# Performance work log

Measured on AMD Instinct MI355X. Metric: run time of the kernel, lower is better.

Reference implementation:

```python
import jax, jax.numpy as jnp
import numpy as np

B, N, C, H = 1, 512, 128, 128  # batch, tokens, pair channels, hidden
ENDING = False
EPS = 1e-5


def _ln(x, w, b):
    m = jnp.mean(x, axis=-1, keepdims=True)
    v = jnp.var(x, axis=-1, keepdims=True)
    return (x - m) * jax.lax.rsqrt(v + EPS) * w + b


def setup_inputs() -> dict:
    key = jax.random.key(0)
    ks = jax.random.split(key, 5)
    s = 0.02  # weight init scale
    return {
        "x": jax.random.normal(ks[0], (B, N, N, C), jnp.float32),
        "norm_in_w": jnp.ones((C,), jnp.float32),
        "norm_in_b": jnp.zeros((C,), jnp.float32),
        "p_in_w": jax.random.normal(ks[1], (2 * H, C), jnp.float32) * s,
        "g_in_w": jax.random.normal(ks[2], (2 * H, C), jnp.float32) * s,
        "norm_out_w": jnp.ones((H,), jnp.float32),
        "norm_out_b": jnp.zeros((H,), jnp.float32),
        "p_out_w": jax.random.normal(ks[3], (C, H), jnp.float32) * s,
        "g_out_w": jax.random.normal(ks[4], (C, C), jnp.float32) * s,
    }


def reference(x, norm_in_w, norm_in_b, p_in_w, g_in_w,
              norm_out_w, norm_out_b, p_out_w, g_out_w):
    # x: [B, N, N, C]
    xn = _ln(x, norm_in_w, norm_in_b)                       # [B,N,N,C]
    h = (xn @ p_in_w.T) * jax.nn.sigmoid(xn @ g_in_w.T)     # [B,N,N,2H]
    a, b = h[..., :H], h[..., H:]
    if ENDING:  # incoming edges
        t = jnp.einsum('bkid,bkjd->bijd', a, b)
    else:       # outgoing edges
        t = jnp.einsum('bikd,bjkd->bijd', a, b)             # [B,N,N,H]
    on = _ln(t, norm_out_w, norm_out_b)
    # NOTE: output gate uses the *input* layernorm activations (xn), per source
    return (on @ p_out_w.T) * jax.nn.sigmoid(xn @ g_out_w.T)  # [B,N,N,C]
```

## Files before the change

### kernel.cpp

```cpp
#include <hip/hip_runtime.h>

typedef short short8 __attribute__((ext_vector_type(8)));
typedef _Float16 half8 __attribute__((ext_vector_type(8)));
typedef float f32x4 __attribute__((ext_vector_type(4)));
typedef unsigned short u16;

#define MFMA16H(a,b,c) __builtin_amdgcn_mfma_f32_16x16x32_f16((a),(b),(c),0,0,0)

__device__ __forceinline__ u16 f2h(float f){
  _Float16 h = (_Float16)f;
  return __builtin_bit_cast(u16, h);
}
__device__ __forceinline__ float h2f(u16 u){
  _Float16 h = __builtin_bit_cast(_Float16, u);
  return (float)h;
}
__device__ __forceinline__ float sigmoidf_(float x){
  return 1.0f / (1.0f + __expf(-x));
}
__device__ __forceinline__ half8 ldh8(const u16* p){ return *(const half8*)p; }

#define PLANE 262144

__global__ __launch_bounds__(256) void prep_w(
    const float* __restrict__ p_in, const float* __restrict__ g_in,
    const float* __restrict__ p_out, const float* __restrict__ g_out,
    u16* __restrict__ wbuf)
{
  int idx = blockIdx.x * 256 + threadIdx.x;
  float v;
  if (idx < 32768)       v = p_in[idx];
  else if (idx < 65536)  v = g_in[idx - 32768];
  else if (idx < 81920)  v = p_out[idx - 65536];
  else                   v = g_out[idx - 81920];
  wbuf[idx] = f2h(v);
}

template<bool S>
__global__ __launch_bounds__(256) void stage1(
    const float* __restrict__ x,
    const float* __restrict__ niw, const float* __restrict__ nib,
    const u16* __restrict__ wbuf,
    u16* __restrict__ a_h, u16* __restrict__ a_l,
    u16* __restrict__ b_h, u16* __restrict__ b_l,
    u16* __restrict__ gate)
{
  __shared__ __align__(16) u16 xnT[64*136];
  __shared__ __align__(16) u16 wp [64*136];
  __shared__ __align__(16) u16 wg [64*136];
  __shared__ __align__(16) u16 hTh[64*72];
  __shared__ __align__(16) u16 hTl[64*72];

  int t = threadIdx.x;
  int p0 = blockIdx.x * 64;
  int i_row = p0 >> 9, k0 = p0 & 511;

  {
    int px = t >> 2, part = t & 3;
    const float* xr = x + (size_t)(p0 + px) * 128 + part * 32;
    float v[32];
    float s = 0.f, ss = 0.f;
#pragma unroll
    for (int q = 0; q < 8; ++q) {
      float4 f = *(const float4*)(xr + q * 4);
      v[q*4+0] = f.x; v[q*4+1] = f.y; v[q*4+2] = f.z; v[q*4+3] = f.w;
      s  += f.x + f.y + f.z + f.w;
      ss += f.x*f.x + f.y*f.y + f.z*f.z + f.w*f.w;
    }
    s  += __shfl_xor(s, 1);  s  += __shfl_xor(s, 2);
    ss += __shfl_xor(ss, 1); ss += __shfl_xor(ss, 2);
    float m  = s * (1.f/128.f);
    float var = ss * (1.f/128.f) - m*m;
    float rs = rsqrtf(var + 1e-5f);
#pragma unroll
    for (int q = 0; q < 4; ++q) {
      short8 o;
#pragma unroll
      for (int j = 0; j < 8; ++j) {
        int c = part*32 + q*8 + j;
        float xv = (v[q*8+j] - m) * rs * niw[c] + nib[c];
        o[j] = (short)f2h(xv);
      }
      *(short8*)&xnT[px*136 + part*32 + q*8] = o;
    }
  }
  __syncthreads();

  int wave = t >> 6, lane = t & 63;
  int fr = lane & 15, hi = lane >> 4;
  int m0 = wave * 16;

  half8 afr[4];
#pragma unroll
  for (int kk = 0; kk < 4; ++kk)
    afr[kk] = ldh8(&xnT[(m0 + fr)*136 + kk*32 + hi*8]);

  for (int ns = 0; ns < 6; ++ns) {
    __syncthreads();
    if (ns < 4) {
      int n0 = ns * 64;
#pragma unroll
      for (int q = 0; q < 4; ++q) {
        int c = t + q*256;
        int row = c >> 4, ko = (c & 15) * 8;
        *(short8*)&wp[row*136 + ko] = *(const short8*)&wbuf[n0*128 + row*128 + ko];
        *(short8*)&wg[row*136 + ko] = *(const short8*)&wbuf[32768 + n0*128 + row*128 + ko];
      }
    } else {
      int n0 = (ns - 4) * 64;
#pragma unroll
      for (int q = 0; q < 4; ++q) {
        int c = t + q*256;
        int row = c >> 4, ko = (c & 15) * 8;
        *(short8*)&wp[row*136 + ko] = *(const short8*)&wbuf[81920 + n0*128 + row*128 + ko];
      }
    }
    __syncthreads();

    f32x4 accP[4] = {}, accG[4] = {};
#pragma unroll
    for (int kk = 0; kk < 4; ++kk) {
#pragma unroll
      for (int nf = 0; nf < 4; ++nf) {
        half8 bp = ldh8(&wp[(nf*16 + fr)*136 + kk*32 + hi*8]);
        accP[nf] = MFMA16H(afr[kk], bp, accP[nf]);
        if (ns < 4) {
          half8 bg = ldh8(&wg[(nf*16 + fr)*136 + kk*32 + hi*8]);
          accG[nf] = MFMA16H(afr[kk], bg, accG[nf]);
        }
      }
    }

    if (ns < 4) {
#pragma unroll
      for (int nf = 0; nf < 4; ++nf) {
#pragma unroll
        for (int r = 0; r < 4; ++r) {
          float h = accP[nf][r] * sigmoidf_(accG[nf][r]);
          int nl = nf*16 + fr;
          int pl = m0 + hi*4 + r;
          u16 hh = f2h(h);
          hTh[nl*72 + pl] = hh;
          if constexpr (S) {
            hTl[nl*72 + pl] = f2h(h - h2f(hh));
          }
        }
      }
      __syncthreads();
      int n0 = ns * 64;
      u16* dh = (ns < 2) ? a_h : b_h;
      u16* dl = (ns < 2) ? a_l : b_l;
      int dbase = (ns < 2) ? n0 : n0 - 128;
      int nl = t >> 2, po = (t & 3) * 16;
      size_t g = (size_t)(dbase + nl) * PLANE + (size_t)i_row * 512 + k0 + po;
      *(short8*)&dh[g]     = *(const short8*)&hTh[nl*72 + po];
      *(short8*)&dh[g + 8] = *(const short8*)&hTh[nl*72 + po + 8];
      if constexpr (S) {
        *(short8*)&dl[g]     = *(const short8*)&hTl[nl*72 + po];
        *(short8*)&dl[g + 8] = *(const short8*)&hTl[nl*72 + po + 8];
      }
    } else {
      int n0 = (ns - 4) * 64;
#pragma unroll
      for (int nf = 0; nf < 4; ++nf) {
#pragma unroll
        for (int r = 0; r < 4; ++r) {
          float gv = sigmoidf_(accP[nf][r]);
          int cc = n0 + nf*16 + fr;
          int pl = m0 + hi*4 + r;
          gate[(size_t)(p0 + pl)*128 + cc] = f2h(gv);
        }
      }
    }
  }
}

template<bool S>
__global__ __launch_bounds__(256) void stage2(
    const u16* __restrict__ a_h, const u16* __restrict__ a_l,
    const u16* __restrict__ b_h, const u16* __restrict__ b_l,
    u16* __restrict__ t_h, u16* __restrict__ t_l)
{
  int bid = blockIdx.x;
  int d  = bid >> 4;
  int it = (bid >> 2) & 3;
  int jt = bid & 3;
  size_t abase = (size_t)d * PLANE + (size_t)it * 128 * 512;
  size_t bbase = (size_t)d * PLANE + (size_t)jt * 128 * 512;

  __shared__ __align__(16) u16 Ash[128*72], Bsh[128*72];
  __shared__ __align__(16) u16 Asl[128*72], Bsl[128*72];

  int t = threadIdx.x, wave = t >> 6, lane = t & 63;
  int fr = lane & 15, hi = lane >> 4;
  int m0 = (wave & 1) * 64, n0 = (wave >> 1) * 64;
  int srow = t >> 1, sko = (t & 1) * 32;

  f32x4 acc[4][4] = {};

  for (int step = 0; step < 8; ++step) {
    __syncthreads();
    int kb = step * 64;
#pragma unroll
    for (int q = 0; q < 4; ++q) {
      size_t go = (size_t)srow*512 + kb + sko + q*8;
      *(short8*)&Ash[srow*72 + sko + q*8] = *(const short8*)&a_h[abase + go];
      *(short8*)&Bsh[srow*72 + sko + q*8] = *(const short8*)&b_h[bbase + go];
      if constexpr (S) {
        *(short8*)&Asl[srow*72 + sko + q*8] = *(const short8*)&a_l[abase + go];
        *(short8*)&Bsl[srow*72 + sko + q*8] = *(const short8*)&b_l[bbase + go];
      }
    }
    __syncthreads();
#pragma unroll
    for (int kk = 0; kk < 2; ++kk) {
      half8 afh[4], bfh[4], afl[4], bfl[4];
#pragma unroll
      for (int mf = 0; mf < 4; ++mf) {
        afh[mf] = ldh8(&Ash[(m0 + mf*16 + fr)*72 + kk*32 + hi*8]);
        if constexpr (S) afl[mf] = ldh8(&Asl[(m0 + mf*16 + fr)*72 + kk*32 + hi*8]);
      }
#pragma unroll
      for (int nf = 0; nf < 4; ++nf) {
        bfh[nf] = ldh8(&Bsh[(n0 + nf*16 + fr)*72 + kk*32 + hi*8]);
        if constexpr (S) bfl[nf] = ldh8(&Bsl[(n0 + nf*16 + fr)*72 + kk*32 + hi*8]);
      }
#pragma unroll
      for (int mf = 0; mf < 4; ++mf)
#pragma unroll
        for (int nf = 0; nf < 4; ++nf) {
          acc[mf][nf] = MFMA16H(afh[mf], bfh[nf], acc[mf][nf]);
          if constexpr (S) {
            acc[mf][nf] = MFMA16H(afh[mf], bfl[nf], acc[mf][nf]);
            acc[mf][nf] = MFMA16H(afl[mf], bfh[nf], acc[mf][nf]);
          }
        }
    }
  }

  u16* Th = t_h + (size_t)d * PLANE;
  u16* Tl = S ? (t_l + (size_t)d * PLANE) : nullptr;
  int ibase = it*128 + m0, jbase = jt*128 + n0;
#pragma unroll
  for (int mf = 0; mf < 4; ++mf)
#pragma unroll
    for (int r = 0; r < 4; ++r) {
      int i = ibase + mf*16 + hi*4 + r;
#pragma unroll
      for (int nf = 0; nf < 4; ++nf) {
        int j = jbase + nf*16 + fr;
        float v = acc[mf][nf][r];
        u16 vh = f2h(v);
        Th[(size_t)i*512 + j] = vh;
        if constexpr (S) Tl[(size_t)i*512 + j] = f2h(v - h2f(vh));
      }
    }
}

template<bool S>
__global__ __launch_bounds__(256) void stage3(
    const u16* __restrict__ t_h, const u16* __restrict__ t_l,
    const u16* __restrict__ gate,
    const float* __restrict__ now_, const float* __restrict__ nob_,
    const u16* __restrict__ wbuf, float* __restrict__ out)
{
  __shared__ __align__(16) u16 tTh[128*72];
  __shared__ __align__(16) u16 tTl[128*72];
  __shared__ __align__(16) u16 onT[64*136];
  __shared__ __align__(16) u16 wpo[128*136];

  int t = threadIdx.x;
  int p0 = blockIdx.x * 64;
  int i_row = p0 >> 9, j0 = p0 & 511;

  {
    int srow = t >> 1, sko = (t & 1) * 32;
#pragma unroll
    for (int q = 0; q < 4; ++q) {
      size_t go = (size_t)srow * PLANE + (size_t)i_row*512 + j0 + sko + q*8;
      *(short8*)&tTh[srow*72 + sko + q*8] = *(const short8*)&t_h[go];
      if constexpr (S)
        *(short8*)&tTl[srow*72 + sko + q*8] = *(const short8*)&t_l[go];
    }
  }
#pragma unroll
  for (int q = 0; q < 8; ++q) {
    int c = t + q*256;
    int row = c >> 4, ko = (c & 15) * 8;
    *(short8*)&wpo[row*136 + ko] = *(const short8*)&wbuf[65536 + row*128 + ko];
  }
  __syncthreads();

  {
    int px = t >> 2, part = t & 3;
    float tv[32]; float s = 0.f, ss = 0.f;
#pragma unroll
    for (int q = 0; q < 32; ++q) {
      int d = part*32 + q;
      float f = h2f(tTh[d*72 + px]);
      if constexpr (S) f += h2f(tTl[d*72 + px]);
      tv[q] = f; s += f; ss += f*f;
    }
    s  += __shfl_xor(s, 1);  s  += __shfl_xor(s, 2);
    ss += __shfl_xor(ss, 1); ss += __shfl_xor(ss, 2);
    float m = s * (1.f/128.f);
    float var = ss * (1.f/128.f) - m*m;
    float rs = rsqrtf(var + 1e-5f);
#pragma unroll
    for (int q = 0; q < 4; ++q) {
      short8 o;
#pragma unroll
      for (int j = 0; j < 8; ++j) {
        int d = part*32 + q*8 + j;
        o[j] = (short)f2h((tv[q*8+j] - m) * rs * now_[d] + nob_[d]);
      }
      *(short8*)&onT[px*136 + part*32 + q*8] = o;
    }
  }
  __syncthreads();

  int wave = t >> 6, lane = t & 63;
  int fr = lane & 15, hi = lane >> 4;
  int m0 = wave * 16;
  half8 af[4];
#pragma unroll
  for (int kk = 0; kk < 4; ++kk)
    af[kk] = ldh8(&onT[(m0 + fr)*136 + kk*32 + hi*8]);
  f32x4 acc[8] = {};
#pragma unroll
  for (int kk = 0; kk < 4; ++kk)
#pragma unroll
    for (int nf = 0; nf < 8; ++nf)
      acc[nf] = MFMA16H(af[kk], ldh8(&wpo[(nf*16 + fr)*136 + kk*32 + hi*8]), acc[nf]);

#pragma unroll
  for (int nf = 0; nf < 8; ++nf)
#pragma unroll
    for (int r = 0; r < 4; ++r) {
      int pl = m0 + hi*4 + r;
      int cc = nf*16 + fr;
      size_t gi = (size_t)(p0 + pl) * 128 + cc;
      out[gi] = acc[nf][r] * h2f(gate[gi]);
    }
}

extern "C" void kernel_launch(void* const* d_in, const int* in_sizes, int n_in,
                              void* d_out, int out_size, void* d_ws, size_t ws_size,
                              hipStream_t stream) {
  const float* x   = (const float*)d_in[0];
  const float* niw = (const float*)d_in[1];
  const float* nib = (const float*)d_in[2];
  const float* piw = (const float*)d_in[3];
  const float* giw = (const float*)d_in[4];
  const float* now_ = (const float*)d_in[5];
  const float* nob_ = (const float*)d_in[6];
  const float* pow_ = (const float*)d_in[7];
  const float* gow  = (const float*)d_in[8];
  float* out = (float*)d_out;

  char* ws = (char*)d_ws;
  const size_t MB = 1048576;
  bool split = ws_size >= (448*MB + 196608);

  if (split) {
    u16* a_h  = (u16*)(ws);
    u16* a_l  = (u16*)(ws + 64*MB);
    u16* b_h  = (u16*)(ws + 128*MB);
    u16* b_l  = (u16*)(ws + 192*MB);
    u16* gate = (u16*)(ws + 256*MB);
    u16* t_h  = (u16*)(ws + 320*MB);
    u16* t_l  = (u16*)(ws + 384*MB);
    u16* wbuf = (u16*)(ws + 448*MB);
    prep_w<<<384, 256, 0, stream>>>(piw, giw, pow_, gow, wbuf);
    stage1<true><<<4096, 256, 0, stream>>>(x, niw, nib, wbuf, a_h, a_l, b_h, b_l, gate);
    stage2<true><<<2048, 256, 0, stream>>>(a_h, a_l, b_h, b_l, t_h, t_l);
    stage3<true><<<4096, 256, 0, stream>>>(t_h, t_l, gate, now_, nob_, wbuf, out);
  } else {
    u16* a_h  = (u16*)(ws);
    u16* b_h  = (u16*)(ws + 64*MB);
    u16* gate = (u16*)(ws + 128*MB);
    u16* t_h  = (u16*)(ws + 192*MB);
    u16* wbuf = (u16*)(ws + 256*MB);
    prep_w<<<384, 256, 0, stream>>>(piw, giw, pow_, gow, wbuf);
    stage1<false><<<4096, 256, 0, stream>>>(x, niw, nib, wbuf, a_h, nullptr, b_h, nullptr, gate);
    stage2<false><<<2048, 256, 0, stream>>>(a_h, nullptr, b_h, nullptr, t_h, nullptr);
    stage3<false><<<4096, 256, 0, stream>>>(t_h, nullptr, gate, now_, nob_, wbuf, out);
  }
}
```

Baseline: 474.4 us.

## Drop t split storage, read weights from global, prefetch stage2 tiles in registers

Several changes land together. Stage1 and stage3 now read weight fragments straight from global memory (L2-cached) instead of staging them into LDS, which removes the barriers and the LDS footprint. Stage1 double-buffers its transpose scratch. Stage2 prefetches the next K tile into registers while storing the current one, sets launch bounds to 2 blocks per CU, and writes only the fp16 high part of t. Dropping the low part of t halves stage2 write and stage3 read traffic but lowers the precision of t before the output layernorm. The non-split fallback path is also removed, so the code now assumes the larger workspace.

```diff
diff --git a/kernel.cpp b/kernel.cpp
--- a/kernel.cpp
+++ b/kernel.cpp
@@ -36,7 +36,6 @@
   wbuf[idx] = f2h(v);
 }
 
-template<bool S>
 __global__ __launch_bounds__(256) void stage1(
     const float* __restrict__ x,
     const float* __restrict__ niw, const float* __restrict__ nib,
@@ -46,10 +45,8 @@
     u16* __restrict__ gate)
 {
   __shared__ __align__(16) u16 xnT[64*136];
-  __shared__ __align__(16) u16 wp [64*136];
-  __shared__ __align__(16) u16 wg [64*136];
-  __shared__ __align__(16) u16 hTh[64*72];
-  __shared__ __align__(16) u16 hTl[64*72];
+  __shared__ __align__(16) u16 hTh[2][64*72];
+  __shared__ __align__(16) u16 hTl[2][64*72];
 
   int t = threadIdx.x;
   int p0 = blockIdx.x * 64;
@@ -96,42 +93,33 @@
     afr[kk] = ldh8(&xnT[(m0 + fr)*136 + kk*32 + hi*8]);
 
   for (int ns = 0; ns < 6; ++ns) {
-    __syncthreads();
+    const u16* wP;
+    const u16* wG = nullptr;
     if (ns < 4) {
       int n0 = ns * 64;
-#pragma unroll
-      for (int q = 0; q < 4; ++q) {
-        int c = t + q*256;
-        int row = c >> 4, ko = (c & 15) * 8;
-        *(short8*)&wp[row*136 + ko] = *(const short8*)&wbuf[n0*128 + row*128 + ko];
-        *(short8*)&wg[row*136 + ko] = *(const short8*)&wbuf[32768 + n0*128 + row*128 + ko];
-      }
+      wP = wbuf + n0*128;
+      wG = wbuf + 32768 + n0*128;
     } else {
       int n0 = (ns - 4) * 64;
-#pragma unroll
-      for (int q = 0; q < 4; ++q) {
-        int c = t + q*256;
-        int row = c >> 4, ko = (c & 15) * 8;
-        *(short8*)&wp[row*136 + ko] = *(const short8*)&wbuf[81920 + n0*128 + row*128 + ko];
-      }
-    }
-    __syncthreads();
+      wP = wbuf + 81920 + n0*128;
+    }
 
     f32x4 accP[4] = {}, accG[4] = {};
 #pragma unroll
     for (int kk = 0; kk < 4; ++kk) {
 #pragma unroll
       for (int nf = 0; nf < 4; ++nf) {
-        half8 bp = ldh8(&wp[(nf*16 + fr)*136 + kk*32 + hi*8]);
+        half8 bp = ldh8(&wP[(nf*16 + fr)*128 + kk*32 + hi*8]);
         accP[nf] = MFMA16H(afr[kk], bp, accP[nf]);
         if (ns < 4) {
-          half8 bg = ldh8(&wg[(nf*16 + fr)*136 + kk*32 + hi*8]);
+          half8 bg = ldh8(&wG[(nf*16 + fr)*128 + kk*32 + hi*8]);
           accG[nf] = MFMA16H(afr[kk], bg, accG[nf]);
         }
       }
     }
 
     if (ns < 4) {
+      int bufi = ns & 1;
 #pragma unroll
       for (int nf = 0; nf < 4; ++nf) {
 #pragma unroll
@@ -140,10 +128,8 @@
           int nl = nf*16 + fr;
           int pl = m0 + hi*4 + r;
           u16 hh = f2h(h);
-          hTh[nl*72 + pl] = hh;
-          if constexpr (S) {
-            hTl[nl*72 + pl] = f2h(h - h2f(hh));
-          }
+          hTh[bufi][nl*72 + pl] = hh;
+          hTl[bufi][nl*72 + pl] = f2h(h - h2f(hh));
         }
       }
       __syncthreads();
@@ -153,12 +139,10 @@
       int dbase = (ns < 2) ? n0 : n0 - 128;
       int nl = t >> 2, po = (t & 3) * 16;
       size_t g = (size_t)(dbase + nl) * PLANE + (size_t)i_row * 512 + k0 + po;
-      *(short8*)&dh[g]     = *(const short8*)&hTh[nl*72 + po];
-      *(short8*)&dh[g + 8] = *(const short8*)&hTh[nl*72 + po + 8];
-      if constexpr (S) {
-        *(short8*)&dl[g]     = *(const short8*)&hTl[nl*72 + po];
-        *(short8*)&dl[g + 8] = *(const short8*)&hTl[nl*72 + po + 8];
-      }
+      *(short8*)&dh[g]     = *(const short8*)&hTh[bufi][nl*72 + po];
+      *(short8*)&dh[g + 8] = *(const short8*)&hTh[bufi][nl*72 + po + 8];
+      *(short8*)&dl[g]     = *(const short8*)&hTl[bufi][nl*72 + po];
+      *(short8*)&dl[g + 8] = *(const short8*)&hTl[bufi][nl*72 + po + 8];
     } else {
       int n0 = (ns - 4) * 64;
 #pragma unroll
@@ -175,11 +159,10 @@
   }
 }
 
-template<bool S>
-__global__ __launch_bounds__(256) void stage2(
+__global__ __launch_bounds__(256, 2) void stage2(
     const u16* __restrict__ a_h, const u16* __restrict__ a_l,
     const u16* __restrict__ b_h, const u16* __restrict__ b_l,
-    u16* __restrict__ t_h, u16* __restrict__ t_l)
+    u16* __restrict__ t_h)
 {
   int bid = blockIdx.x;
   int d  = bid >> 4;
@@ -197,18 +180,35 @@
   int srow = t >> 1, sko = (t & 1) * 32;
 
   f32x4 acc[4][4] = {};
+  short8 rah[4], ral[4], rbh[4], rbl[4];
+
+#pragma unroll
+  for (int q = 0; q < 4; ++q) {
+    size_t go = (size_t)srow*512 + sko + q*8;
+    rah[q] = *(const short8*)&a_h[abase + go];
+    ral[q] = *(const short8*)&a_l[abase + go];
+    rbh[q] = *(const short8*)&b_h[bbase + go];
+    rbl[q] = *(const short8*)&b_l[bbase + go];
+  }
 
   for (int step = 0; step < 8; ++step) {
     __syncthreads();
-    int kb = step * 64;
 #pragma unroll
     for (int q = 0; q < 4; ++q) {
-      size_t go = (size_t)srow*512 + kb + sko + q*8;
-      *(short8*)&Ash[srow*72 + sko + q*8] = *(const short8*)&a_h[abase + go];
-      *(short8*)&Bsh[srow*72 + sko + q*8] = *(const short8*)&b_h[bbase + go];
-      if constexpr (S) {
-        *(short8*)&Asl[srow*72 + sko + q*8] = *(const short8*)&a_l[abase + go];
-        *(short8*)&Bsl[srow*72 + sko + q*8] = *(const short8*)&b_l[bbase + go];
+      *(short8*)&Ash[srow*72 + sko + q*8] = rah[q];
+      *(short8*)&Asl[srow*72 + sko + q*8] = ral[q];
+      *(short8*)&Bsh[srow*72 + sko + q*8] = rbh[q];
+      *(short8*)&Bsl[srow*72 + sko + q*8] = rbl[q];
+    }
+    if (step < 7) {
+      int kb = (step + 1) * 64;
+#pragma unroll
+      for (int q = 0; q < 4; ++q) {
+        size_t go = (size_t)srow*512 + kb + sko + q*8;
+        rah[q] = *(const short8*)&a_h[abase + go];
+        ral[q] = *(const short8*)&a_l[abase + go];
+        rbh[q] = *(const short8*)&b_h[bbase + go];
+        rbl[q] = *(const short8*)&b_l[bbase + go];
       }
     }
     __syncthreads();
@@ -218,28 +218,25 @@
 #pragma unroll
       for (int mf = 0; mf < 4; ++mf) {
         afh[mf] = ldh8(&Ash[(m0 + mf*16 + fr)*72 + kk*32 + hi*8]);
-        if constexpr (S) afl[mf] = ldh8(&Asl[(m0 + mf*16 + fr)*72 + kk*32 + hi*8]);
+        afl[mf] = ldh8(&Asl[(m0 + mf*16 + fr)*72 + kk*32 + hi*8]);
       }
 #pragma unroll
       for (int nf = 0; nf < 4; ++nf) {
         bfh[nf] = ldh8(&Bsh[(n0 + nf*16 + fr)*72 + kk*32 + hi*8]);
-        if constexpr (S) bfl[nf] = ldh8(&Bsl[(n0 + nf*16 + fr)*72 + kk*32 + hi*8]);
+        bfl[nf] = ldh8(&Bsl[(n0 + nf*16 + fr)*72 + kk*32 + hi*8]);
       }
 #pragma unroll
       for (int mf = 0; mf < 4; ++mf)
 #pragma unroll
         for (int nf = 0; nf < 4; ++nf) {
           acc[mf][nf] = MFMA16H(afh[mf], bfh[nf], acc[mf][nf]);
-          if constexpr (S) {
-            acc[mf][nf] = MFMA16H(afh[mf], bfl[nf], acc[mf][nf]);
-            acc[mf][nf] = MFMA16H(afl[mf], bfh[nf], acc[mf][nf]);
-          }
+          acc[mf][nf] = MFMA16H(afh[mf], bfl[nf], acc[mf][nf]);
+          acc[mf][nf] = MFMA16H(afl[mf], bfh[nf], acc[mf][nf]);
         }
     }
   }
 
-  u16* Th = t_h + (size_t)d * PLANE;
-  u16* Tl = S ? (t_l + (size_t)d * PLANE) : nullptr;
+  u16* T = t_h + (size_t)d * PLANE;
   int ibase = it*128 + m0, jbase = jt*128 + n0;
 #pragma unroll
   for (int mf = 0; mf < 4; ++mf)
@@ -249,25 +246,18 @@
 #pragma unroll
       for (int nf = 0; nf < 4; ++nf) {
         int j = jbase + nf*16 + fr;
-        float v = acc[mf][nf][r];
-        u16 vh = f2h(v);
-        Th[(size_t)i*512 + j] = vh;
-        if constexpr (S) Tl[(size_t)i*512 + j] = f2h(v - h2f(vh));
-      }
-    }
-}
-
-template<bool S>
+        T[(size_t)i*512 + j] = f2h(acc[mf][nf][r]);
+      }
+    }
+}
+
 __global__ __launch_bounds__(256) void stage3(
-    const u16* __restrict__ t_h, const u16* __restrict__ t_l,
-    const u16* __restrict__ gate,
+    const u16* __restrict__ t_h, const u16* __restrict__ gate,
     const float* __restrict__ now_, const float* __restrict__ nob_,
     const u16* __restrict__ wbuf, float* __restrict__ out)
 {
   __shared__ __align__(16) u16 tTh[128*72];
-  __shared__ __align__(16) u16 tTl[128*72];
   __shared__ __align__(16) u16 onT[64*136];
-  __shared__ __align__(16) u16 wpo[128*136];
 
   int t = threadIdx.x;
   int p0 = blockIdx.x * 64;
@@ -276,18 +266,9 @@
   {
     int srow = t >> 1, sko = (t & 1) * 32;
 #pragma unroll
-    for (int q = 0; q < 4; ++q) {
-      size_t go = (size_t)srow * PLANE + (size_t)i_row*512 + j0 + sko + q*8;
-      *(short8*)&tTh[srow*72 + sko + q*8] = *(const short8*)&t_h[go];
-      if constexpr (S)
-        *(short8*)&tTl[srow*72 + sko + q*8] = *(const short8*)&t_l[go];
-    }
-  }
-#pragma unroll
-  for (int q = 0; q < 8; ++q) {
-    int c = t + q*256;
-    int row = c >> 4, ko = (c & 15) * 8;
-    *(short8*)&wpo[row*136 + ko] = *(const short8*)&wbuf[65536 + row*128 + ko];
+    for (int q = 0; q < 4; ++q)
+      *(short8*)&tTh[srow*72 + sko + q*8] =
+        *(const short8*)&t_h[(size_t)srow * PLANE + (size_t)i_row*512 + j0 + sko + q*8];
   }
   __syncthreads();
 
@@ -298,7 +279,6 @@
     for (int q = 0; q < 32; ++q) {
       int d = part*32 + q;
       float f = h2f(tTh[d*72 + px]);
-      if constexpr (S) f += h2f(tTl[d*72 + px]);
       tv[q] = f; s += f; ss += f*f;
     }
     s  += __shfl_xor(s, 1);  s  += __shfl_xor(s, 2);
@@ -326,12 +306,13 @@
 #pragma unroll
   for (int kk = 0; kk < 4; ++kk)
     af[kk] = ldh8(&onT[(m0 + fr)*136 + kk*32 + hi*8]);
+  const u16* wpo = wbuf + 65536;
   f32x4 acc[8] = {};
 #pragma unroll
   for (int kk = 0; kk < 4; ++kk)
 #pragma unroll
     for (int nf = 0; nf < 8; ++nf)
-      acc[nf] = MFMA16H(af[kk], ldh8(&wpo[(nf*16 + fr)*136 + kk*32 + hi*8]), acc[nf]);
+      acc[nf] = MFMA16H(af[kk], ldh8(&wpo[(nf*16 + fr)*128 + kk*32 + hi*8]), acc[nf]);
 
 #pragma unroll
   for (int nf = 0; nf < 8; ++nf)
@@ -360,30 +341,16 @@
 
   char* ws = (char*)d_ws;
   const size_t MB = 1048576;
-  bool split = ws_size >= (448*MB + 196608);
-
-  if (split) {
-    u16* a_h  = (u16*)(ws);
-    u16* a_l  = (u16*)(ws + 64*MB);
-    u16* b_h  = (u16*)(ws + 128*MB);
-    u16* b_l  = (u16*)(ws + 192*MB);
-    u16* gate = (u16*)(ws + 256*MB);
-    u16* t_h  = (u16*)(ws + 320*MB);
-    u16* t_l  = (u16*)(ws + 384*MB);
-    u16* wbuf = (u16*)(ws + 448*MB);
-    prep_w<<<384, 256, 0, stream>>>(piw, giw, pow_, gow, wbuf);
-    stage1<true><<<4096, 256, 0, stream>>>(x, niw, nib, wbuf, a_h, a_l, b_h, b_l, gate);
-    stage2<true><<<2048, 256, 0, stream>>>(a_h, a_l, b_h, b_l, t_h, t_l);
-    stage3<true><<<4096, 256, 0, stream>>>(t_h, t_l, gate, now_, nob_, wbuf, out);
-  } else {
-    u16* a_h  = (u16*)(ws);
-    u16* b_h  = (u16*)(ws + 64*MB);
-    u16* gate = (u16*)(ws + 128*MB);
-    u16* t_h  = (u16*)(ws + 192*MB);
-    u16* wbuf = (u16*)(ws + 256*MB);
-    prep_w<<<384, 256, 0, stream>>>(piw, giw, pow_, gow, wbuf);
-    stage1<false><<<4096, 256, 0, stream>>>(x, niw, nib, wbuf, a_h, nullptr, b_h, nullptr, gate);
-    stage2<false><<<2048, 256, 0, stream>>>(a_h, nullptr, b_h, nullptr, t_h, nullptr);
-    stage3<false><<<4096, 256, 0, stream>>>(t_h, nullptr, gate, now_, nob_, wbuf, out);
-  }
-}
+  u16* a_h  = (u16*)(ws);
+  u16* a_l  = (u16*)(ws + 64*MB);
+  u16* b_h  = (u16*)(ws + 128*MB);
+  u16* b_l  = (u16*)(ws + 192*MB);
+  u16* gate = (u16*)(ws + 256*MB);
+  u16* t_h  = (u16*)(ws + 320*MB);
+  u16* wbuf = (u16*)(ws + 384*MB);
+
+  prep_w<<<384, 256, 0, stream>>>(piw, giw, pow_, gow, wbuf);
+  stage1<<<4096, 256, 0, stream>>>(x, niw, nib, wbuf, a_h, a_l, b_h, b_l, gate);
+  stage2<<<2048, 256, 0, stream>>>(a_h, a_l, b_h, b_l, t_h);
+  stage3<<<4096, 256, 0, stream>>>(t_h, gate, now_, nob_, wbuf, out);
+}
```

After: 652.6 us. 37.6% more time.
